# Kernel optimization log

Measured on AMD Instinct MI355X. Metric: run time of the kernel, lower is better.

Reference implementation:

```python
import jax, jax.numpy as jnp
import numpy as np

K = 9           # kernel_size * dilation (dilation=1 -> stride-1 slice is identity)
BN_EPS = 1e-5   # fresh BatchNorm2d (eval): running_mean=0, running_var=1
L2_EPS = 1e-12  # torch F.normalize eps


def setup_inputs() -> dict:
    key = jax.random.key(0)
    k1, k2 = jax.random.split(key, 2)
    B, C, H, W = 4, 192, 56, 56
    Cout = 384
    x = jax.random.normal(k1, (B, C, H, W), jnp.float32)
    conv_w = jax.random.normal(k2, (Cout, 2 * C), jnp.float32) * 0.05  # 1x1 conv weight
    conv_b = jnp.zeros((Cout,), jnp.float32)
    bn_gamma = jnp.ones((Cout,), jnp.float32)
    bn_beta = jnp.zeros((Cout,), jnp.float32)
    return dict(x=x, conv_w=conv_w, conv_b=conv_b, bn_gamma=bn_gamma, bn_beta=bn_beta)


def _knn_idx(xf, k):
    """xf: (B,C,N). L2-normalize channels, pairwise sq-dist, top-k nearest. -> (B,N,k) int32."""
    xn = xf / jnp.maximum(jnp.linalg.norm(xf, axis=1, keepdims=True), L2_EPS)
    pts = xn.transpose(0, 2, 1)                       # (B,N,C)
    sq = jnp.sum(pts * pts, axis=-1)                  # (B,N)
    dist = sq[:, :, None] - 2.0 * jnp.einsum('bnc,bmc->bnm', pts, pts) + sq[:, None, :]
    _, idx = jax.lax.top_k(-dist, k)                  # smallest distance first
    return idx


def reference(x, conv_w, conv_b, bn_gamma, bn_beta):
    B, C, H, W = x.shape
    N = H * W
    xf = x.reshape(B, C, N)                           # (B,C,N,1) squeezed
    nn_idx = _knn_idx(jax.lax.stop_gradient(xf), K)   # KNN built under no_grad

    xt = xf.transpose(0, 2, 1)                        # (B,N,C)
    x_j = jax.vmap(lambda f, i: f[i])(xt, nn_idx)     # (B,N,K,C) neighbor gather
    x_i = jnp.broadcast_to(xt[:, :, None, :], (B, N, K, C))
    feat = jnp.concatenate([x_i, x_j - x_i], axis=-1)  # (B,N,K,2C) edge features

    # BasicConv: 1x1 conv + BatchNorm2d (eval, mean=0,var=1) + GELU
    z = jnp.einsum('bnkc,oc->bnko', feat, conv_w) + conv_b
    z = z * (bn_gamma / np.sqrt(1.0 + BN_EPS)) + bn_beta
    z = jax.nn.gelu(z, approximate=False)

    out = jnp.max(z, axis=2)                          # max over K neighbors -> (B,N,O)
    out = out.transpose(0, 2, 1).reshape(B, -1, H, W)

    center = jnp.broadcast_to(jnp.arange(N, dtype=nn_idx.dtype)[None, :, None], (B, N, K))
    edge_index = jnp.stack([nn_idx, center], axis=0)  # (2,B,N,K), debug=True output
    return out, edge_index
```

## Files before the change

### kernel.cpp

```cpp
#include <hip/hip_runtime.h>
#include <hip/hip_bf16.h>
#include <math.h>

#define B_    4
#define C_    192
#define NPT   3136
#define CO_   384
#define KNN   9
#define CAND  64
#define NROWS (B_*NPT)
#define SD    10

typedef _Float16 half8 __attribute__((ext_vector_type(8)));
typedef float    f32x4 __attribute__((ext_vector_type(4)));

__device__ __forceinline__ float u2f(unsigned short u) {
    unsigned int t = ((unsigned int)u) << 16;
    float f; __builtin_memcpy(&f, &t, 4); return f;
}
__device__ __forceinline__ unsigned short f2u(float f) {
    __hip_bfloat16 h = __float2bfloat16(f);
    unsigned short u; __builtin_memcpy(&u, &h, 2); return u;
}
__device__ __forceinline__ float gelu_exact(float y) {
    return 0.5f * y * (1.0f + erff(y * 0.70710678118654752f));
}
__device__ __forceinline__ unsigned long long dkey(double d) {
    long long sb = __double_as_longlong(d);
    unsigned long long u = (unsigned long long)sb;
    return (sb < 0) ? ~u : (u | 0x8000000000000000ULL);
}

__global__ __launch_bounds__(256) void k_norm(
    const float* __restrict__ x,
    float* __restrict__ invn32, double* __restrict__ invn64,
    double* __restrict__ sqd, float* __restrict__ nrm32)
{
    __shared__ double part[4][64];
    int wave = threadIdx.x >> 6, lane = threadIdx.x & 63;
    int p0 = blockIdx.x * 64;
    int row = p0 + lane;
    int b = row / NPT, n = row % NPT;
    const float* xb = x + (size_t)b * C_ * NPT + n;
    double S = 0.0;
    int c0 = wave * 48;
    for (int c = c0; c < c0 + 48; ++c) {
        double v = (double)xb[(size_t)c * NPT];
        S = fma(v, v, S);
    }
    part[wave][lane] = S;
    __syncthreads();
    if (threadIdx.x < 64) {
        double T = ((part[0][lane] + part[1][lane]) + part[2][lane])
                 + part[3][lane];
        double nrm = sqrt(T);
        if (nrm < 1e-12) nrm = 1e-12;
        double iv = 1.0 / nrm;
        int prow = p0 + lane;
        invn64[prow] = iv;
        invn32[prow] = (float)iv;
        sqd[prow] = iv * iv * T;
        nrm32[prow] = (float)nrm;
    }
}

__global__ __launch_bounds__(256) void k_xpose(
    const float* __restrict__ x, float* __restrict__ xT,
    const float* __restrict__ invn32, _Float16* __restrict__ packed)
{
    __shared__ float t[32][33];
    int blk = blockIdx.x;
    int b  = blk / 588;
    int r  = blk % 588;
    int ct = r / 98, nt = r % 98;
    int c0 = ct * 32, n0 = nt * 32;
    int tid = threadIdx.x;
    int tx = tid & 31, ty8 = tid >> 5;
    const float* xb = x + (size_t)b * C_ * NPT;
#pragma unroll
    for (int e = 0; e < 4; ++e) {
        int cc = ty8 + e * 8;
        t[cc][tx] = xb[(size_t)(c0 + cc) * NPT + n0 + tx];
    }
    __syncthreads();
#pragma unroll
    for (int e = 0; e < 4; ++e) {
        int nn = ty8 + e * 8;
        xT[(size_t)(b * NPT + n0 + nn) * C_ + c0 + tx] = t[tx][nn];
    }
    if (tid < 128) {
        int f = tid >> 6, l = tid & 63;
        int pt = f * 16 + (l & 15);
        float iv = invn32[(size_t)b * NPT + n0 + pt];
        int cb = (l >> 4) * 8;
        half8 h;
#pragma unroll
        for (int e = 0; e < 8; ++e)
            h[e] = (_Float16)(t[cb + e][pt] * iv);
        size_t idx = ((((size_t)(b * 196 + nt * 2 + f)) * 6 + ct) * 64 + l) * 8;
        *(half8*)(packed + idx) = h;
    }
}

__global__ __launch_bounds__(256) void k_wpack(
    const float* __restrict__ cw, _Float16* __restrict__ wpk)
{
    int t = blockIdx.x * 256 + threadIdx.x;
    if (t >= 48 * 6 * 64) return;
    int l  = t & 63;
    int tk = t >> 6;
    int kk = tk % 6, ot = tk / 6;
    int hsel = ot / 24;
    int o = (ot % 24) * 16 + (l & 15);
    int k = kk * 32 + (l >> 4) * 8;
    half8 h;
#pragma unroll
    for (int e = 0; e < 8; ++e) {
        float w2 = cw[(size_t)o * 384 + C_ + k + e];
        float wv = hsel ? w2 : (cw[(size_t)o * 384 + k + e] - w2);
        h[e] = (_Float16)wv;
    }
    *(half8*)(wpk + (size_t)t * 8) = h;
}

__global__ __launch_bounds__(256) void k_screen_mfma(
    const _Float16* __restrict__ packed, unsigned short* __restrict__ cand)
{
    __shared__ unsigned md[64][4 * SD + 1];
    int blk   = blockIdx.x;
    int chunk = blk / 196;
    int t2    = blk % 196;
    int b     = t2 / 49;
    int itile = t2 % 49;
    int tid   = threadIdx.x;
    int wave  = tid >> 6, lane = tid & 63;
    int it    = itile * 4 + wave;

    const _Float16* pb = packed + ((size_t)(b * 196 + it) * 6) * 512 + lane * 8;
    half8 bf[6];
#pragma unroll
    for (int kk = 0; kk < 6; ++kk)
        bf[kk] = *(const half8*)(pb + kk * 512);

    int jt0 = chunk * 28;
    const int ntj = 28;

    unsigned bd[SD];
#pragma unroll
    for (int q = 0; q < SD; ++q) bd[q] = 0u;

    const _Float16* pa_base =
        packed + ((size_t)(b * 196 + jt0) * 6) * 512 + lane * 8;

    half8 af[6];
#pragma unroll
    for (int kk = 0; kk < 6; ++kk)
        af[kk] = *(const half8*)(pa_base + kk * 512);

    for (int jt = 0; jt < ntj; ++jt) {
        f32x4 acc = {0.f, 0.f, 0.f, 0.f};
#pragma unroll
        for (int kk = 0; kk < 6; ++kk)
            acc = __builtin_amdgcn_mfma_f32_16x16x32_f16(af[kk], bf[kk], acc, 0, 0, 0);

        if (jt + 1 < ntj) {
            const _Float16* pn = pa_base + (size_t)(jt + 1) * 6 * 512;
#pragma unroll
            for (int kk = 0; kk < 6; ++kk)
                af[kk] = *(const half8*)(pn + kk * 512);
        }

        unsigned jb = (unsigned)((jt0 + jt) * 16 + (lane >> 4) * 4);
#pragma unroll
        for (int q = 0; q < 4; ++q) {
            float s = acc[q] + 2.0f;
            unsigned fb = __float_as_uint(s);
            unsigned c = (fb & 0xFFFFF000u) | (jb + (unsigned)q);
#pragma unroll
            for (int t = 0; t < SD; ++t) {
                unsigned old = bd[t];
                unsigned mx = old > c ? old : c;
                c           = old > c ? c : old;
                bd[t] = mx;
            }
        }
    }

    int ir = wave * 16 + (lane & 15);
    int g  = lane >> 4;
#pragma unroll
    for (int q = 0; q < SD; ++q) md[ir][g * SD + q] = bd[q];
    __syncthreads();

    if (tid < 64) {
        int h[4] = {0, 0, 0, 0};
        unsigned short* cp =
            cand + ((size_t)b * NPT + itile * 64 + tid) * CAND + chunk * 9;
        const unsigned* rd = &md[tid][0];
        for (int s = 0; s < 9; ++s) {
            unsigned best = 0u; int bg = 0;
#pragma unroll
            for (int g2 = 0; g2 < 4; ++g2) {
                unsigned v = (h[g2] < SD) ? rd[g2 * SD + h[g2]] : 0u;
                if (v > best) { best = v; bg = g2; }
            }
            cp[s] = (unsigned short)(best & 0xFFFu);
            h[bg]++;
        }
        if (chunk == 0)
            cand[((size_t)b * NPT + itile * 64 + tid) * CAND + 63] = 0;
    }
}

__global__ __launch_bounds__(256) void k_refine(
    const float* __restrict__ xT, const double* __restrict__ invn64,
    const double* __restrict__ sqd, const unsigned short* __restrict__ cand,
    float* __restrict__ e0)
{
    __shared__ unsigned long long kbuf[4][CAND];
    __shared__ int    icand[4][CAND];
    __shared__ double civ[4][CAND];
    __shared__ double csq[4][CAND];
    __shared__ float  xi[4][C_];
    int wave = threadIdx.x >> 6;
    int lane = threadIdx.x & 63;
    int row  = blockIdx.x * 4 + wave;
    int b    = row / NPT;
    size_t bN = (size_t)b * NPT;

    int jc = (int)cand[(size_t)row * CAND + lane];
    icand[wave][lane] = jc;
    civ[wave][lane] = invn64[bN + jc];
    csq[wave][lane] = sqd[bN + jc];
    const float* xiRow = xT + (size_t)row * C_;
    xi[wave][lane]       = xiRow[lane];
    xi[wave][lane + 64]  = xiRow[lane + 64];
    xi[wave][lane + 128] = xiRow[lane + 128];
    __syncthreads();

    int sub = lane & 7, cg = lane >> 3;
    double ivi = invn64[row], sqi = sqd[row];
    const float* xw = &xi[wave][sub * 4];

    float4 h0a, h0b, h0c;
    {
        int j0 = icand[wave][cg];
        const float* p = xT + (bN + j0) * C_ + sub * 4;
        h0a = *(const float4*)&p[0];
        h0b = *(const float4*)&p[32];
        h0c = *(const float4*)&p[64];
    }

#pragma unroll
    for (int cc = 0; cc < 8; ++cc) {
        int cidx = cc * 8 + cg;
        int jcur = icand[wave][cidx];
        const float* pc = xT + (bN + jcur) * C_ + sub * 4;
        float4 h1a = *(const float4*)&pc[96];
        float4 h1b = *(const float4*)&pc[128];
        float4 h1c = *(const float4*)&pc[160];

        double d0 = 0.0, d1 = 0.0, d2 = 0.0, d3 = 0.0;
        {
            float4 xq;
            xq = *(const float4*)&xw[0];
            d0 = fma((double)xq.x, (double)h0a.x, d0);
            d1 = fma((double)xq.y, (double)h0a.y, d1);
            d2 = fma((double)xq.z, (double)h0a.z, d2);
            d3 = fma((double)xq.w, (double)h0a.w, d3);
            xq = *(const float4*)&xw[32];
            d0 = fma((double)xq.x, (double)h0b.x, d0);
            d1 = fma((double)xq.y, (double)h0b.y, d1);
            d2 = fma((double)xq.z, (double)h0b.z, d2);
            d3 = fma((double)xq.w, (double)h0b.w, d3);
            xq = *(const float4*)&xw[64];
            d0 = fma((double)xq.x, (double)h0c.x, d0);
            d1 = fma((double)xq.y, (double)h0c.y, d1);
            d2 = fma((double)xq.z, (double)h0c.z, d2);
            d3 = fma((double)xq.w, (double)h0c.w, d3);
        }
        if (cc < 7) {
            int jn = icand[wave][cidx + 8];
            const float* pn = xT + (bN + jn) * C_ + sub * 4;
            h0a = *(const float4*)&pn[0];
            h0b = *(const float4*)&pn[32];
            h0c = *(const float4*)&pn[64];
        }
        {
            float4 xq;
            xq = *(const float4*)&xw[96];
            d0 = fma((double)xq.x, (double)h1a.x, d0);
            d1 = fma((double)xq.y, (double)h1a.y, d1);
            d2 = fma((double)xq.z, (double)h1a.z, d2);
            d3 = fma((double)xq.w, (double)h1a.w, d3);
            xq = *(const float4*)&xw[128];
            d0 = fma((double)xq.x, (double)h1b.x, d0);
            d1 = fma((double)xq.y, (double)h1b.y, d1);
            d2 = fma((double)xq.z, (double)h1b.z, d2);
            d3 = fma((double)xq.w, (double)h1b.w, d3);
            xq = *(const float4*)&xw[160];
            d0 = fma((double)xq.x, (double)h1c.x, d0);
            d1 = fma((double)xq.y, (double)h1c.y, d1);
            d2 = fma((double)xq.z, (double)h1c.z, d2);
            d3 = fma((double)xq.w, (double)h1c.w, d3);
        }
        double dot = (d0 + d1) + (d2 + d3);
        dot += __shfl_xor(dot, 1);
        dot += __shfl_xor(dot, 2);
        dot += __shfl_xor(dot, 4);
        if (sub == 0) {
            double dist = sqi + csq[wave][cidx]
                        - 2.0 * (ivi * civ[wave][cidx] * dot);
            kbuf[wave][cidx] = dkey(dist);
        }
    }
    if (lane == 0) kbuf[wave][63] = 0xFFFFFFFFFFFFFFFFULL;
    __syncthreads();

    unsigned long long kd = kbuf[wave][lane];
    int jme = icand[wave][lane];
    int rank = 0;
#pragma unroll
    for (int m = 0; m < CAND; ++m) {
        unsigned long long km = kbuf[wave][m];
        int jm = icand[wave][m];
        rank += ((km < kd) || (km == kd && jm < jme)) ? 1 : 0;
    }
    if (rank < KNN)
        e0[(size_t)row * KNN + rank] = (float)jme;
}

__global__ __launch_bounds__(256) void k_gemm_mfma(
    const _Float16* __restrict__ packed, const _Float16* __restrict__ wpk,
    const float* __restrict__ nrm32, const float* __restrict__ cb,
    unsigned short* __restrict__ Bh, float* __restrict__ Zf)
{
    int pt   = blockIdx.x;
    int wave = threadIdx.x >> 6, lane = threadIdx.x & 63;
    int hsel = wave >> 1;
    int og   = wave & 1;

    const _Float16* px = packed + (size_t)pt * 6 * 512 + lane * 8;
    half8 pf[6];
#pragma unroll
    for (int kk = 0; kk < 6; ++kk) pf[kk] = *(const half8*)(px + kk * 512);

    float s = nrm32[pt * 16 + (lane & 15)];
    size_t row0 = (size_t)pt * 16 + (lane & 15);
    int olane = (lane >> 4) * 4;

    int ot0 = hsel * 24 + og * 12;
    const _Float16* wb = wpk + (size_t)ot0 * 6 * 512 + lane * 8;

    half8 wf[6];
#pragma unroll
    for (int kk = 0; kk < 6; ++kk) wf[kk] = *(const half8*)(wb + kk * 512);

    for (int t = 0; t < 12; ++t) {
        f32x4 acc = {0.f, 0.f, 0.f, 0.f};
#pragma unroll
        for (int kk = 0; kk < 6; ++kk)
            acc = __builtin_amdgcn_mfma_f32_16x16x32_f16(wf[kk], pf[kk], acc, 0, 0, 0);

        if (t < 11) {
            const _Float16* wn = wb + (size_t)(t + 1) * 6 * 512;
#pragma unroll
            for (int kk = 0; kk < 6; ++kk)
                wf[kk] = *(const half8*)(wn + kk * 512);
        }

        int o = (og * 12 + t) * 16 + olane;
        if (hsel == 0) {
            float4 cbv = *(const float4*)&cb[o];
            float4 zv;
            zv.x = acc[0] * s + cbv.x; zv.y = acc[1] * s + cbv.y;
            zv.z = acc[2] * s + cbv.z; zv.w = acc[3] * s + cbv.w;
            *(float4*)&Zf[row0 * 384 + o] = zv;
        } else {
            ushort4 pk;
            pk.x = f2u(acc[0] * s); pk.y = f2u(acc[1] * s);
            pk.z = f2u(acc[2] * s); pk.w = f2u(acc[3] * s);
            *(ushort4*)&Bh[row0 * 384 + o] = pk;
        }
    }
}

__global__ __launch_bounds__(256) void k_out2(
    const float* __restrict__ e0, const float* __restrict__ gam,
    const float* __restrict__ bet, float* __restrict__ out,
    const unsigned short* __restrict__ Bh, const float* __restrict__ Zf)
{
    __shared__ int jidx[64 * KNN];
    int blk = blockIdx.x;
    int b   = blk / 294;
    int r   = blk % 294;
    int nt  = r % 49, ot = r / 49;
    int n0 = nt * 64, o0 = ot * 64;
    int tid = threadIdx.x;
    int tx = tid & 15, ty = tid >> 4;

    for (int e = tid; e < 64 * KNN; e += 256)
        jidx[e] = (int)e0[((size_t)b * NPT + n0 + e / KNN) * KNN + e % KNN];

    const float inv_s = 0.9999950000374997f;
    float gs[4], bts[4];
#pragma unroll
    for (int v = 0; v < 4; ++v) {
        int o = o0 + tx * 4 + v;
        gs[v]  = gam[o] * inv_s;
        bts[v] = bet[o];
    }
    __syncthreads();

    float best[4][4];
#pragma unroll
    for (int u = 0; u < 4; ++u) {
        float4 z = *(const float4*)
            &Zf[(size_t)(b * NPT + n0 + ty * 4 + u) * 384 + o0 + tx * 4];
        float zA[4] = {z.x, z.y, z.z, z.w};

        float ymin[4], ymax[4];
#pragma unroll
        for (int v = 0; v < 4; ++v) { ymin[v] = 1e30f; ymax[v] = -1e30f; }

        const int* jr = &jidx[(ty * 4 + u) * KNN];
#pragma unroll
        for (int k = 0; k < KNN; ++k) {
            int j = jr[k];
            ushort4 g = *(const ushort4*)
                &Bh[(size_t)(b * NPT + j) * 384 + o0 + tx * 4];
            float bvv[4] = {u2f(g.x), u2f(g.y), u2f(g.z), u2f(g.w)};
#pragma unroll
            for (int v = 0; v < 4; ++v) {
                float y = fmaf(zA[v] + bvv[v], gs[v], bts[v]);
                ymin[v] = fminf(ymin[v], y);
                ymax[v] = fmaxf(ymax[v], y);
            }
        }
#pragma unroll
        for (int v = 0; v < 4; ++v)
            best[u][v] = fmaxf(gelu_exact(ymin[v]), gelu_exact(ymax[v]));
    }

#pragma unroll
    for (int v = 0; v < 4; ++v) {
        int o = o0 + tx * 4 + v;
        float4 pk = {best[0][v], best[1][v], best[2][v], best[3][v]};
        *(float4*)(out + ((size_t)(b * CO_ + o)) * NPT + n0 + ty * 4) = pk;
    }
}

__global__ __launch_bounds__(256) void k_gemmB(
    const float* __restrict__ x, const float* __restrict__ cw,
    void* __restrict__ Bq, int bbase, int bcol0, int ldB, int storeBf16,
    int botiles, int bstrideBytes)
{
    int per = 49 * botiles;
    int blk = blockIdx.x;
    int bi  = blk / per;
    int r   = blk % per;
    int b   = bbase + bi;
    int bm = r % 49;
    int bo = r / 49;
    int m0 = bm * 64;
    char* Bp = (char*)Bq + (size_t)bi * (size_t)bstrideBytes;

    __shared__ float Xt[16][68];
    __shared__ float Wt[16][68];
    int tid = threadIdx.x;
    int tx = tid & 15, ty = tid >> 4;
    const float* xb = x + (size_t)b * C_ * NPT;
    float acc[4][4];
#pragma unroll
    for (int u = 0; u < 4; ++u)
#pragma unroll
        for (int v = 0; v < 4; ++v) acc[u][v] = 0.f;

    for (int ct = 0; ct < 12; ++ct) {
        int c0 = ct * 16;
        {
            int cc = tid >> 4, n4 = (tid & 15) * 4;
            *(float4*)&Xt[cc][n4] =
                *(const float4*)&xb[(size_t)(c0 + cc) * NPT + m0 + n4];
        }
        {
            int oo = tid >> 2, c4 = (tid & 3) * 4;
            int o = bcol0 + bo * 64 + oo;
            float4 w = *(const float4*)&cw[(size_t)o * 384 + C_ + c0 + c4];
            Wt[c4 + 0][oo] = w.x; Wt[c4 + 1][oo] = w.y;
            Wt[c4 + 2][oo] = w.z; Wt[c4 + 3][oo] = w.w;
        }
        __syncthreads();
#pragma unroll
        for (int cc = 0; cc < 16; ++cc) {
            float4 av = *(const float4*)&Xt[cc][ty * 4];
            float4 bv = *(const float4*)&Wt[cc][tx * 4];
            float a_[4] = {av.x, av.y, av.z, av.w};
            float b_[4] = {bv.x, bv.y, bv.z, bv.w};
#pragma unroll
            for (int u = 0; u < 4; ++u)
#pragma unroll
                for (int v = 0; v < 4; ++v)
                    acc[u][v] = fmaf(a_[u], b_[v], acc[u][v]);
        }
        __syncthreads();
    }
    if (!storeBf16) {
        float* Bf = (float*)Bp;
#pragma unroll
        for (int u = 0; u < 4; ++u) {
            float4 pk = {acc[u][0], acc[u][1], acc[u][2], acc[u][3]};
            *(float4*)&Bf[(size_t)(m0 + ty * 4 + u) * ldB + bo * 64 + tx * 4] = pk;
        }
    } else {
        unsigned short* Bh = (unsigned short*)Bp;
#pragma unroll
        for (int u = 0; u < 4; ++u) {
            ushort4 pk;
            pk.x = f2u(acc[u][0]); pk.y = f2u(acc[u][1]);
            pk.z = f2u(acc[u][2]); pk.w = f2u(acc[u][3]);
            *(ushort4*)&Bh[(size_t)(m0 + ty * 4 + u) * ldB + bo * 64 + tx * 4] = pk;
        }
    }
}

__global__ __launch_bounds__(256) void k_outA(
    const float* __restrict__ x, const float* __restrict__ cw,
    const float* __restrict__ e0, const float* __restrict__ cb,
    const float* __restrict__ gam, const float* __restrict__ bet,
    float* __restrict__ out, const void* __restrict__ Bq,
    int bbase, int o0base, int bcol0, int ldB, int readBf16,
    int botiles, int bstrideBytes)
{
    int per = 49 * botiles;
    int blk = blockIdx.x;
    int bi  = blk / per;
    int r   = blk % per;
    int b   = bbase + bi;
    int nt = r % 49, ot = r / 49;
    int n0 = nt * 64, o0 = o0base + ot * 64;
    const char* Bp = (const char*)Bq + (size_t)bi * (size_t)bstrideBytes;

    __shared__ float Xi[16][68];
    __shared__ float Wd[16][68];
    __shared__ int jidx[64 * KNN];
    int tid = threadIdx.x;
    int tx = tid & 15, ty = tid >> 4;
    const float* xb = x + (size_t)b * C_ * NPT;

    for (int e = tid; e < 64 * KNN; e += 256)
        jidx[e] = (int)e0[((size_t)b * NPT + n0 + e / KNN) * KNN + e % KNN];

    float zA[4][4];
#pragma unroll
    for (int u = 0; u < 4; ++u)
#pragma unroll
        for (int v = 0; v < 4; ++v) zA[u][v] = 0.f;

    for (int ct = 0; ct < 12; ++ct) {
        int c0 = ct * 16;
        {
            int cc = tid >> 4, n4 = (tid & 15) * 4;
            *(float4*)&Xi[cc][n4] =
                *(const float4*)&xb[(size_t)(c0 + cc) * NPT + n0 + n4];
        }
        {
            int oo = tid >> 2, c4 = (tid & 3) * 4;
            int o = o0 + oo;
            float4 w1 = *(const float4*)&cw[(size_t)o * 384 + c0 + c4];
            float4 w2 = *(const float4*)&cw[(size_t)o * 384 + C_ + c0 + c4];
            Wd[c4 + 0][oo] = w1.x - w2.x; Wd[c4 + 1][oo] = w1.y - w2.y;
            Wd[c4 + 2][oo] = w1.z - w2.z; Wd[c4 + 3][oo] = w1.w - w2.w;
        }
        __syncthreads();
#pragma unroll
        for (int cc = 0; cc < 16; ++cc) {
            float4 av = *(const float4*)&Xi[cc][ty * 4];
            float4 bv = *(const float4*)&Wd[cc][tx * 4];
            float a_[4] = {av.x, av.y, av.z, av.w};
            float b_[4] = {bv.x, bv.y, bv.z, bv.w};
#pragma unroll
            for (int u = 0; u < 4; ++u)
#pragma unroll
                for (int v = 0; v < 4; ++v)
                    zA[u][v] = fmaf(a_[u], b_[v], zA[u][v]);
        }
        __syncthreads();
    }

    const float inv_s = 0.9999950000374997f;
    float gs[4], bts[4], cbs[4];
#pragma unroll
    for (int v = 0; v < 4; ++v) {
        int o = o0 + tx * 4 + v;
        gs[v]  = gam[o] * inv_s;
        bts[v] = bet[o];
        cbs[v] = cb[o];
    }

    float best[4][4];
#pragma unroll
    for (int u = 0; u < 4; ++u)
#pragma unroll
        for (int v = 0; v < 4; ++v) best[u][v] = -1e30f;

    int obB = o0 - bcol0;
    for (int k = 0; k < KNN; ++k) {
#pragma unroll
        for (int u = 0; u < 4; ++u) {
            int j = jidx[(ty * 4 + u) * KNN + k];
            float bvv[4];
            if (!readBf16) {
                float4 g = *(const float4*)
                    ((const float*)Bp + (size_t)j * ldB + obB + tx * 4);
                bvv[0] = g.x; bvv[1] = g.y; bvv[2] = g.z; bvv[3] = g.w;
            } else {
                ushort4 g = *(const ushort4*)
                    ((const unsigned short*)Bp + (size_t)j * ldB + obB + tx * 4);
                bvv[0] = u2f(g.x); bvv[1] = u2f(g.y);
                bvv[2] = u2f(g.z); bvv[3] = u2f(g.w);
            }
#pragma unroll
            for (int v = 0; v < 4; ++v) {
                float z = zA[u][v] + bvv[v] + cbs[v];
                float y = fmaf(z, gs[v], bts[v]);
                float ge = 0.5f * y * (1.0f + erff(y * 0.70710678118654752f));
                best[u][v] = fmaxf(best[u][v], ge);
            }
        }
    }

#pragma unroll
    for (int v = 0; v < 4; ++v) {
        int o = o0 + tx * 4 + v;
        float4 pk = {best[0][v], best[1][v], best[2][v], best[3][v]};
        *(float4*)(out + ((size_t)(b * CO_ + o)) * NPT + n0 + ty * 4) = pk;
    }
}

__global__ __launch_bounds__(256) void k_center(float* __restrict__ e1)
{
    int p = blockIdx.x * 256 + threadIdx.x;
    if (p >= NROWS * KNN) return;
    e1[p] = (float)((p / KNN) % NPT);
}

extern "C" void kernel_launch(void* const* d_in, const int* in_sizes, int n_in,
                              void* d_out, int out_size, void* d_ws, size_t ws_size,
                              hipStream_t stream)
{
    const float* x   = (const float*)d_in[0];
    const float* cw  = (const float*)d_in[1];
    const float* cb  = (const float*)d_in[2];
    const float* gam = (const float*)d_in[3];
    const float* bet = (const float*)d_in[4];

    float* ou   = (float*)d_out;
    float* out0 = ou;
    double* invn64 = (double*)d_out;
    double* sqd    = (double*)((char*)d_out + 100352);
    float*  invn32 = (float*)((char*)d_out + 200704);
    unsigned short* cand =
        (unsigned short*)((char*)d_out + 250880);
    _Float16* packed = (_Float16*)(ou + 464128);
    float*    nrm32  = (float*)((char*)d_out + 6673408);
    _Float16* wpk    = (_Float16*)((char*)d_out + 6723584);
    float* xT = ou + 2408448;
    float* e0 = ou + 4816896;
    float* e1 = ou + 4929792;

    k_norm       <<<NROWS / 64, 256, 0, stream>>>(x, invn32, invn64, sqd, nrm32);
    k_xpose      <<<B_ * 6 * 98, 256, 0, stream>>>(x, xT, invn32, packed);
    k_screen_mfma<<<7 * B_ * 49, 256, 0, stream>>>(packed, cand);
    k_refine     <<<NROWS / 4, 256, 0, stream>>>(xT, invn64, sqd, cand, e0);

    const size_t BH_BYTES = (size_t)NROWS * 384 * 2;
    const size_t ZF_BYTES = (size_t)NROWS * 384 * 4;
    const int    BSTRIDE  = NPT * CO_ * 4;

    if (ws_size >= BH_BYTES + ZF_BYTES) {
        unsigned short* wsB = (unsigned short*)d_ws;
        float* wsZ = (float*)((char*)d_ws + BH_BYTES);
        k_wpack    <<<72, 256, 0, stream>>>(cw, wpk);
        k_gemm_mfma<<<784, 256, 0, stream>>>(packed, wpk, nrm32, cb, wsB, wsZ);
        k_out2     <<<B_ * 49 * 6, 256, 0, stream>>>(e0, gam, bet, out0,
                                                     wsB, wsZ);
    } else if (ws_size >= ZF_BYTES) {
        k_gemmB<<<B_ * 49 * 6, 256, 0, stream>>>(
            x, cw, d_ws, 0, 0, 384, 0, 6, BSTRIDE);
        k_outA <<<B_ * 49 * 6, 256, 0, stream>>>(
            x, cw, e0, cb, gam, bet, out0, (const void*)d_ws,
            0, 0, 0, 384, 0, 6, BSTRIDE);
    } else {
        k_gemmB<<<2 * 49 * 6, 256, 0, stream>>>(
            x, cw, (void*)ou, 2, 0, 384, 0, 6, BSTRIDE);
        k_outA <<<2 * 49 * 6, 256, 0, stream>>>(
            x, cw, e0, cb, gam, bet, out0, (const void*)ou,
            2, 0, 0, 384, 0, 6, BSTRIDE);
        k_gemmB<<<49 * 6, 256, 0, stream>>>(
            x, cw, (void*)ou, 1, 0, 384, 0, 6, 0);
        k_outA <<<49 * 6, 256, 0, stream>>>(
            x, cw, e0, cb, gam, bet, out0, (const void*)ou,
            1, 0, 0, 384, 0, 6, 0);
        k_gemmB<<<49 * 3, 256, 0, stream>>>(
            x, cw, (void*)ou, 0, 192, 192, 1, 3, 0);
        k_outA <<<49 * 3, 256, 0, stream>>>(
            x, cw, e0, cb, gam, bet, out0, (const void*)ou,
            0, 192, 192, 192, 1, 3, 0);
        k_gemmB<<<49 * 2, 256, 0, stream>>>(
            x, cw, (void*)ou, 0, 64, 128, 1, 2, 0);
        k_outA <<<49 * 2, 256, 0, stream>>>(
            x, cw, e0, cb, gam, bet, out0, (const void*)ou,
            0, 64, 64, 128, 1, 2, 0);
        k_gemmB<<<49 * 1, 256, 0, stream>>>(
            x, cw, (void*)e1, 0, 0, 64, 1, 1, 0);
        k_outA <<<49 * 1, 256, 0, stream>>>(
            x, cw, e0, cb, gam, bet, out0, (const void*)e1,
            0, 0, 0, 64, 1, 1, 0);
    }
    k_center<<<(NROWS * KNN + 255) / 256, 256, 0, stream>>>(e1);
}
```

Before: 207.5 us.

## Pre-rank screen candidates by approximate key and refine only the top 24

The screening kernel now stores the full 32-bit approximate-distance key with each candidate instead of only the index. The refine kernel ranks the 63 candidates by that key and runs the exact double-precision distance only on the best 24, which cuts gather traffic and FP64 work by about two thirds. The center-index output write is folded into k_out2, removing a separate kernel launch. The trade-off is that a true neighbor could be missed if the fp16 screen ranks it below 24th, and twice as much candidate data is written to the scratch area.

```diff
diff --git a/kernel.cpp b/kernel.cpp
--- a/kernel.cpp
+++ b/kernel.cpp
@@ -7,7 +7,7 @@
 #define NPT   3136
 #define CO_   384
 #define KNN   9
-#define CAND  64
+#define K2    24
 #define NROWS (B_*NPT)
 #define SD    10
 
@@ -124,7 +124,7 @@
 }
 
 __global__ __launch_bounds__(256) void k_screen_mfma(
-    const _Float16* __restrict__ packed, unsigned short* __restrict__ cand)
+    const _Float16* __restrict__ packed, unsigned* __restrict__ cand)
 {
     __shared__ unsigned md[64][4 * SD + 1];
     int blk   = blockIdx.x;
@@ -194,8 +194,8 @@
 
     if (tid < 64) {
         int h[4] = {0, 0, 0, 0};
-        unsigned short* cp =
-            cand + ((size_t)b * NPT + itile * 64 + tid) * CAND + chunk * 9;
+        size_t rowi = (size_t)b * NPT + itile * 64 + tid;
+        unsigned* cp = cand + rowi * 64 + chunk * 9;
         const unsigned* rd = &md[tid][0];
         for (int s = 0; s < 9; ++s) {
             unsigned best = 0u; int bg = 0;
@@ -204,23 +204,24 @@
                 unsigned v = (h[g2] < SD) ? rd[g2 * SD + h[g2]] : 0u;
                 if (v > best) { best = v; bg = g2; }
             }
-            cp[s] = (unsigned short)(best & 0xFFFu);
+            cp[s] = best;
             h[bg]++;
         }
         if (chunk == 0)
-            cand[((size_t)b * NPT + itile * 64 + tid) * CAND + 63] = 0;
+            cand[rowi * 64 + 63] = 0u;
     }
 }
 
 __global__ __launch_bounds__(256) void k_refine(
     const float* __restrict__ xT, const double* __restrict__ invn64,
-    const double* __restrict__ sqd, const unsigned short* __restrict__ cand,
+    const double* __restrict__ sqd, const unsigned* __restrict__ cand32,
     float* __restrict__ e0)
 {
-    __shared__ unsigned long long kbuf[4][CAND];
-    __shared__ int    icand[4][CAND];
-    __shared__ double civ[4][CAND];
-    __shared__ double csq[4][CAND];
+    __shared__ unsigned km[4][64];
+    __shared__ int    icand[4][K2];
+    __shared__ double civ[4][K2];
+    __shared__ double csq[4][K2];
+    __shared__ unsigned long long kbuf[4][K2];
     __shared__ float  xi[4][C_];
     int wave = threadIdx.x >> 6;
     int lane = threadIdx.x & 63;
@@ -228,14 +229,26 @@
     int b    = row / NPT;
     size_t bN = (size_t)b * NPT;
 
-    int jc = (int)cand[(size_t)row * CAND + lane];
-    icand[wave][lane] = jc;
-    civ[wave][lane] = invn64[bN + jc];
-    csq[wave][lane] = sqd[bN + jc];
+    unsigned kc = cand32[(size_t)row * 64 + lane];
+    km[wave][lane] = kc;
     const float* xiRow = xT + (size_t)row * C_;
     xi[wave][lane]       = xiRow[lane];
     xi[wave][lane + 64]  = xiRow[lane + 64];
     xi[wave][lane + 128] = xiRow[lane + 128];
+    __syncthreads();
+
+    int keyrank = 0;
+#pragma unroll
+    for (int m = 0; m < 64; ++m)
+        keyrank += (km[wave][m] > kc) ? 1 : 0;
+    if (keyrank < K2)
+        icand[wave][keyrank] = (int)(kc & 0xFFFu);
+    __syncthreads();
+    if (lane < K2) {
+        int j = icand[wave][lane];
+        civ[wave][lane] = invn64[bN + j];
+        csq[wave][lane] = sqd[bN + j];
+    }
     __syncthreads();
 
     int sub = lane & 7, cg = lane >> 3;
@@ -252,7 +265,7 @@
     }
 
 #pragma unroll
-    for (int cc = 0; cc < 8; ++cc) {
+    for (int cc = 0; cc < K2 / 8; ++cc) {
         int cidx = cc * 8 + cg;
         int jcur = icand[wave][cidx];
         const float* pc = xT + (bN + jcur) * C_ + sub * 4;
@@ -279,7 +292,7 @@
             d2 = fma((double)xq.z, (double)h0c.z, d2);
             d3 = fma((double)xq.w, (double)h0c.w, d3);
         }
-        if (cc < 7) {
+        if (cc < K2 / 8 - 1) {
             int jn = icand[wave][cidx + 8];
             const float* pn = xT + (bN + jn) * C_ + sub * 4;
             h0a = *(const float4*)&pn[0];
@@ -314,20 +327,21 @@
             kbuf[wave][cidx] = dkey(dist);
         }
     }
-    if (lane == 0) kbuf[wave][63] = 0xFFFFFFFFFFFFFFFFULL;
     __syncthreads();
 
-    unsigned long long kd = kbuf[wave][lane];
-    int jme = icand[wave][lane];
-    int rank = 0;
-#pragma unroll
-    for (int m = 0; m < CAND; ++m) {
-        unsigned long long km = kbuf[wave][m];
-        int jm = icand[wave][m];
-        rank += ((km < kd) || (km == kd && jm < jme)) ? 1 : 0;
-    }
-    if (rank < KNN)
-        e0[(size_t)row * KNN + rank] = (float)jme;
+    if (lane < K2) {
+        unsigned long long kd = kbuf[wave][lane];
+        int jme = icand[wave][lane];
+        int rank = 0;
+#pragma unroll
+        for (int m = 0; m < K2; ++m) {
+            unsigned long long km2 = kbuf[wave][m];
+            int jm = icand[wave][m];
+            rank += ((km2 < kd) || (km2 == kd && jm < jme)) ? 1 : 0;
+        }
+        if (rank < KNN)
+            e0[(size_t)row * KNN + rank] = (float)jme;
+    }
 }
 
 __global__ __launch_bounds__(256) void k_gemm_mfma(
@@ -388,7 +402,8 @@
 __global__ __launch_bounds__(256) void k_out2(
     const float* __restrict__ e0, const float* __restrict__ gam,
     const float* __restrict__ bet, float* __restrict__ out,
-    const unsigned short* __restrict__ Bh, const float* __restrict__ Zf)
+    const unsigned short* __restrict__ Bh, const float* __restrict__ Zf,
+    float* __restrict__ e1)
 {
     __shared__ int jidx[64 * KNN];
     int blk = blockIdx.x;
@@ -401,6 +416,11 @@
 
     for (int e = tid; e < 64 * KNN; e += 256)
         jidx[e] = (int)e0[((size_t)b * NPT + n0 + e / KNN) * KNN + e % KNN];
+
+    {
+        int p = blk * 96 + tid;
+        if (tid < 96) e1[p] = (float)((p / KNN) % NPT);
+    }
 
     const float inv_s = 0.9999950000374997f;
     float gs[4], bts[4];
@@ -660,19 +680,18 @@
     double* invn64 = (double*)d_out;
     double* sqd    = (double*)((char*)d_out + 100352);
     float*  invn32 = (float*)((char*)d_out + 200704);
-    unsigned short* cand =
-        (unsigned short*)((char*)d_out + 250880);
-    _Float16* packed = (_Float16*)(ou + 464128);
-    float*    nrm32  = (float*)((char*)d_out + 6673408);
-    _Float16* wpk    = (_Float16*)((char*)d_out + 6723584);
+    unsigned* cand32 = (unsigned*)((char*)d_out + 250880);
+    _Float16* packed = (_Float16*)((char*)d_out + 3462144);
+    float*    nrm32  = (float*)((char*)d_out + 8279040);
+    _Float16* wpk    = (_Float16*)((char*)d_out + 8329216);
     float* xT = ou + 2408448;
     float* e0 = ou + 4816896;
     float* e1 = ou + 4929792;
 
     k_norm       <<<NROWS / 64, 256, 0, stream>>>(x, invn32, invn64, sqd, nrm32);
     k_xpose      <<<B_ * 6 * 98, 256, 0, stream>>>(x, xT, invn32, packed);
-    k_screen_mfma<<<7 * B_ * 49, 256, 0, stream>>>(packed, cand);
-    k_refine     <<<NROWS / 4, 256, 0, stream>>>(xT, invn64, sqd, cand, e0);
+    k_screen_mfma<<<7 * B_ * 49, 256, 0, stream>>>(packed, cand32);
+    k_refine     <<<NROWS / 4, 256, 0, stream>>>(xT, invn64, sqd, cand32, e0);
 
     const size_t BH_BYTES = (size_t)NROWS * 384 * 2;
     const size_t ZF_BYTES = (size_t)NROWS * 384 * 4;
@@ -684,13 +703,14 @@
         k_wpack    <<<72, 256, 0, stream>>>(cw, wpk);
         k_gemm_mfma<<<784, 256, 0, stream>>>(packed, wpk, nrm32, cb, wsB, wsZ);
         k_out2     <<<B_ * 49 * 6, 256, 0, stream>>>(e0, gam, bet, out0,
-                                                     wsB, wsZ);
+                                                     wsB, wsZ, e1);
     } else if (ws_size >= ZF_BYTES) {
         k_gemmB<<<B_ * 49 * 6, 256, 0, stream>>>(
             x, cw, d_ws, 0, 0, 384, 0, 6, BSTRIDE);
         k_outA <<<B_ * 49 * 6, 256, 0, stream>>>(
             x, cw, e0, cb, gam, bet, out0, (const void*)d_ws,
             0, 0, 0, 384, 0, 6, BSTRIDE);
+        k_center<<<(NROWS * KNN + 255) / 256, 256, 0, stream>>>(e1);
     } else {
         k_gemmB<<<2 * 49 * 6, 256, 0, stream>>>(
             x, cw, (void*)ou, 2, 0, 384, 0, 6, BSTRIDE);
@@ -717,6 +737,6 @@
         k_outA <<<49 * 1, 256, 0, stream>>>(
             x, cw, e0, cb, gam, bet, out0, (const void*)e1,
             0, 0, 0, 64, 1, 1, 0);
-    }
-    k_center<<<(NROWS * KNN + 255) / 256, 256, 0, stream>>>(e1);
-}
+        k_center<<<(NROWS * KNN + 255) / 256, 256, 0, stream>>>(e1);
+    }
+}
```

Measured after the change: 188.5 us. 9.2% less time.
